# Optimization experiments

Hardware: AMD Instinct MI355X
Metric: run time of the kernel (lower is better)

## Reference

```python
import jax, jax.numpy as jnp
import numpy as np

N_NODES = 50000
W_IN = 256
W_OUT = 256
HEADS = 8
D_HEAD = W_OUT // HEADS
NUM_EDGE = 3
N_EDGES = 800000
NEG_SLOPE = 0.2


def setup_inputs() -> dict:
    key = jax.random.key(0)
    ks = jax.random.split(key, 10)
    x = jax.random.normal(ks[0], (N_NODES, W_IN), dtype=jnp.float32)
    adj = jax.random.randint(ks[1], (NUM_EDGE, 2, N_EDGES), 0, N_NODES, dtype=jnp.int64)
    sw = 1.0 / np.sqrt(W_IN)
    # Per-edge-type GATConv params, stacked on leading edge-type axis
    Ws = jax.random.normal(ks[2], (NUM_EDGE, W_IN, HEADS * D_HEAD), dtype=jnp.float32) * sw
    a_l = jax.random.normal(ks[3], (NUM_EDGE, HEADS, D_HEAD), dtype=jnp.float32) * 0.1
    a_r = jax.random.normal(ks[4], (NUM_EDGE, HEADS, D_HEAD), dtype=jnp.float32) * 0.1
    bias = jnp.zeros((NUM_EDGE, HEADS * D_HEAD), dtype=jnp.float32)
    # Semantic attention layer: Linear(w_out -> 1)
    att_w = jax.random.normal(ks[5], (W_OUT, 1), dtype=jnp.float32) * (1.0 / np.sqrt(W_OUT))
    att_b = jnp.zeros((1,), dtype=jnp.float32)
    return {"x": x, "adj": adj, "Ws": Ws, "a_l": a_l, "a_r": a_r,
            "bias": bias, "att_w": att_w, "att_b": att_b}


def _gat(x, edge_index, W, al, ar, b):
    # x: [N, W_IN]; edge_index: [2, E]; W: [W_IN, H*D]; al/ar: [H, D]; b: [H*D]
    N = x.shape[0]
    h = (x @ W).reshape(N, HEADS, D_HEAD)            # [N, H, D]
    src, dst = edge_index[0], edge_index[1]
    el = jnp.einsum('nhd,hd->nh', h, al)             # src-side scores [N, H]
    er = jnp.einsum('nhd,hd->nh', h, ar)             # dst-side scores [N, H]
    e = jax.nn.leaky_relu(el[src] + er[dst], NEG_SLOPE)   # [E, H]
    # segment softmax over incoming edges of each dst node
    m = jax.ops.segment_max(e, dst, num_segments=N)       # [N, H]
    e = jnp.exp(e - m[dst])
    s = jax.ops.segment_sum(e, dst, num_segments=N)       # [N, H]
    alpha = e / (s[dst] + 1e-9)                           # [E, H]
    out = jax.ops.segment_sum(alpha[:, :, None] * h[src], dst, num_segments=N)
    return out.reshape(N, HEADS * D_HEAD) + b             # concat heads [N, W_OUT]


def reference(x, adj, Ws, a_l, a_r, bias, att_w, att_b):
    outs = [_gat(x, adj[i], Ws[i], a_l[i], a_r[i], bias[i]) for i in range(NUM_EDGE)]
    stacked = jnp.stack(outs, axis=1)                     # [N, T, W_OUT]
    # AttentionLayer: scores = Linear(stacked) viewed as [N, 1, T]; NO softmax (faithful)
    att = (stacked @ att_w + att_b).reshape(-1, 1, NUM_EDGE)  # [N, 1, T]
    return jnp.matmul(att, stacked).squeeze(1)            # [N, W_OUT]
```

## Files before the change

### kernel.cpp

```cpp
#include <hip/hip_runtime.h>

#define N_NODES 50000
#define W_IN    256
#define W_OUT   256
#define HEADS   8
#define NUM_T   3
#define N_EDGES 800000
#define NEG_SLOPE 0.2f

#define NB      128
#define BSH     9
#define BNODES  512
#define P1_EPT  16
#define P1_CHUNK (256 * P1_EPT)
#define P1_BLOCKS ((N_EDGES + P1_CHUNK - 1) / P1_CHUNK)
#define NB_USED ((N_NODES + BNODES - 1) / BNODES)

typedef __attribute__((ext_vector_type(8))) short bf16x8;
typedef __attribute__((ext_vector_type(4))) float f32x4;

__device__ __forceinline__ unsigned short f2b(float f) {
    unsigned u = __float_as_uint(f);
    u = (u + 0x7fffu + ((u >> 16) & 1u)) >> 16;
    return (unsigned short)u;
}
__device__ __forceinline__ float blo(unsigned u) { return __uint_as_float(u << 16); }
__device__ __forceinline__ float bhi(unsigned u) { return __uint_as_float(u & 0xffff0000u); }

__global__ __launch_bounds__(256) void convert_x(const float* __restrict__ x,
                                                 unsigned short* __restrict__ xb) {
    const size_t i = ((size_t)blockIdx.x * 256 + threadIdx.x) * 4;
    const float4 v = *(const float4*)(x + i);
    ushort4 o;
    o.x = f2b(v.x); o.y = f2b(v.y); o.z = f2b(v.z); o.w = f2b(v.w);
    *(ushort4*)(xb + i) = o;
}

__global__ __launch_bounds__(256) void convert_W(const float* __restrict__ Wsrc,
                                                 unsigned short* __restrict__ Wt) {
    const int t = blockIdx.y;
    const int gid = blockIdx.x * 256 + threadIdx.x;
    const int k = gid >> 8, n = gid & 255;
    Wt[(size_t)t * 65536 + (size_t)n * 256 + k] = f2b(Wsrc[(size_t)t * 65536 + gid]);
}

__global__ __launch_bounds__(256) void p1_hist(const int* __restrict__ adj,
                                               int* __restrict__ bucket_cnt) {
    __shared__ int lh[NB];
    const int t = blockIdx.y;
    const int tid = threadIdx.x;
    if (tid < NB) lh[tid] = 0;
    __syncthreads();

    const int* dstp = adj + (size_t)t * 2 * N_EDGES + N_EDGES;
    const int e0 = blockIdx.x * P1_CHUNK + tid * P1_EPT;
#pragma unroll
    for (int i = 0; i < P1_EPT; ++i) {
        const int e = e0 + i;
        if (e < N_EDGES) atomicAdd(&lh[dstp[e] >> BSH], 1);
    }
    __syncthreads();
    if (tid < NB && lh[tid] > 0) atomicAdd(&bucket_cnt[t * NB + tid], lh[tid]);
}

__global__ __launch_bounds__(128) void p1_scan(const int* __restrict__ bucket_cnt,
                                               int* __restrict__ bucket_ptr,
                                               int* __restrict__ bucket_cur) {
    __shared__ int s[NB];
    const int tid = threadIdx.x;
    for (int t = 0; t < NUM_T; ++t) {
        const int v = bucket_cnt[t * NB + tid];
        s[tid] = v;
        __syncthreads();
        for (int off = 1; off < NB; off <<= 1) {
            int o = (tid >= off) ? s[tid - off] : 0;
            __syncthreads();
            s[tid] += o;
            __syncthreads();
        }
        const int incl = s[tid];
        const int excl = incl - v;
        bucket_ptr[t * (NB + 1) + tid] = excl;
        bucket_cur[t * NB + tid] = excl;
        if (tid == NB - 1) bucket_ptr[t * (NB + 1) + NB] = incl;
        __syncthreads();
    }
}

__global__ __launch_bounds__(256) void p1_scatter(const int* __restrict__ adj,
                                                  int* __restrict__ bucket_cur,
                                                  uint2* __restrict__ part) {
    __shared__ int lh[NB];
    __shared__ int lbase[NB];
    const int t = blockIdx.y;
    const int tid = threadIdx.x;
    if (tid < NB) lh[tid] = 0;
    __syncthreads();

    const int* srcp = adj + (size_t)t * 2 * N_EDGES;
    const int* dstp = srcp + N_EDGES;
    const int e0 = blockIdx.x * P1_CHUNK + tid * P1_EPT;

    int es[P1_EPT], ed[P1_EPT], rk[P1_EPT];
#pragma unroll
    for (int i = 0; i < P1_EPT; ++i) {
        const int e = e0 + i;
        if (e < N_EDGES) {
            es[i] = srcp[e];
            ed[i] = dstp[e];
            rk[i] = atomicAdd(&lh[ed[i] >> BSH], 1);
        } else {
            ed[i] = -1;
        }
    }
    __syncthreads();
    if (tid < NB && lh[tid] > 0)
        lbase[tid] = atomicAdd(&bucket_cur[t * NB + tid], lh[tid]);
    __syncthreads();

    uint2* pt = part + (size_t)t * N_EDGES;
#pragma unroll
    for (int i = 0; i < P1_EPT; ++i) {
        if (ed[i] >= 0) {
            const int b = ed[i] >> BSH;
            pt[lbase[b] + rk[i]] = make_uint2((unsigned)es[i], (unsigned)ed[i]);
        }
    }
}

__global__ __launch_bounds__(256) void p2_csr(const uint2* __restrict__ part,
                                              const int* __restrict__ bucket_ptr,
                                              int* __restrict__ row_ptr_all,
                                              int* __restrict__ csr_all) {
    __shared__ int sc[BNODES];
    const int b = blockIdx.x;
    const int t = blockIdx.y;
    const int tid = threadIdx.x;
    const int lane = tid & 63;
    const int wave = tid >> 6;

    const uint2* pt = part + (size_t)t * N_EDGES;
    int* row_ptr = row_ptr_all + (size_t)t * (N_NODES + 1);
    int* csr = csr_all + (size_t)t * N_EDGES;

    const int bp0 = bucket_ptr[t * (NB + 1) + b];
    const int bp1 = bucket_ptr[t * (NB + 1) + b + 1];
    const int node0 = b * BNODES;
    int nn = N_NODES - node0; if (nn > BNODES) nn = BNODES;

    sc[tid] = 0; sc[tid + 256] = 0;
    __syncthreads();

    for (int idx = bp0 + tid; idx < bp1; idx += 256)
        atomicAdd(&sc[pt[idx].y - node0], 1);
    __syncthreads();

    if (wave == 0) {
        int v[8], ex[8];
        int s = 0;
#pragma unroll
        for (int i = 0; i < 8; ++i) { v[i] = sc[lane * 8 + i]; ex[i] = s; s += v[i]; }
        int run = s;
        for (int off = 1; off < 64; off <<= 1) {
            int o = __shfl_up(run, off);
            if (lane >= off) run += o;
        }
        const int base = run - s;
#pragma unroll
        for (int i = 0; i < 8; ++i) sc[lane * 8 + i] = base + ex[i];
    }
    __syncthreads();

    for (int i = tid; i < nn; i += 256) row_ptr[node0 + i] = bp0 + sc[i];
    if (b == NB_USED - 1 && tid == 0) row_ptr[N_NODES] = N_EDGES;
    __syncthreads();

    for (int idx = bp0 + tid; idx < bp1; idx += 256) {
        const uint2 e = pt[idx];
        const int pos = bp0 + atomicAdd(&sc[e.y - node0], 1);
        csr[pos] = (int)e.x;
    }
}

__global__ __launch_bounds__(256) void gemm_fused(const unsigned short* __restrict__ xb,
                                                  const unsigned short* __restrict__ Wt,
                                                  const float* __restrict__ al,
                                                  const float* __restrict__ ar,
                                                  unsigned short* __restrict__ H,
                                                  float* __restrict__ el,
                                                  float* __restrict__ er) {
    __shared__ unsigned short As[64 * 40];
    __shared__ unsigned short Bs[256 * 40];
    __shared__ float els[64 * 8];
    __shared__ float ers[64 * 8];

    const int tid = threadIdx.x;
    const int wave = tid >> 6;
    const int lane = tid & 63;
    const int quad = lane >> 4;
    const int l16 = lane & 15;
    const int m0 = blockIdx.x * 64;

    f32x4 acc[4][4] = {};

    const int arow = tid >> 2;
    const int achunk = (tid & 3) * 8;
    int gm = m0 + arow;
    if (gm > N_NODES - 1) gm = N_NODES - 1;
    const unsigned short* aptr = xb + (size_t)gm * W_IN + achunk;

    for (int k0 = 0; k0 < W_IN; k0 += 32) {
        const uint4 av = *(const uint4*)(aptr + k0);
        *(uint4*)&As[arow * 40 + achunk] = av;
#pragma unroll
        for (int i = 0; i < 4; ++i) {
            const int idx = i * 256 + tid;
            const int brow = idx >> 2;
            const int bch = (idx & 3) * 8;
            const uint4 bv = *(const uint4*)(Wt + (size_t)brow * W_IN + k0 + bch);
            *(uint4*)&Bs[brow * 40 + bch] = bv;
        }
        __syncthreads();

        bf16x8 af[4], bfr[4];
#pragma unroll
        for (int mi = 0; mi < 4; ++mi)
            af[mi] = *(const bf16x8*)&As[(mi * 16 + l16) * 40 + quad * 8];
#pragma unroll
        for (int ni = 0; ni < 4; ++ni)
            bfr[ni] = *(const bf16x8*)&Bs[(wave * 64 + ni * 16 + l16) * 40 + quad * 8];
#pragma unroll
        for (int mi = 0; mi < 4; ++mi)
#pragma unroll
            for (int ni = 0; ni < 4; ++ni)
                acc[mi][ni] = __builtin_amdgcn_mfma_f32_16x16x32_bf16(
                    af[mi], bfr[ni], acc[mi][ni], 0, 0, 0);
        __syncthreads();
    }

#pragma unroll
    for (int mi = 0; mi < 4; ++mi)
#pragma unroll
        for (int reg = 0; reg < 4; ++reg) {
            const int gr = m0 + mi * 16 + quad * 4 + reg;
            if (gr < N_NODES)
#pragma unroll
                for (int ni = 0; ni < 4; ++ni)
                    H[(size_t)gr * W_OUT + wave * 64 + ni * 16 + l16] =
                        f2b(acc[mi][ni][reg]);
        }

    float al4[4], ar4[4];
#pragma unroll
    for (int ni = 0; ni < 4; ++ni) {
        const int c = wave * 64 + ni * 16 + l16;
        al4[ni] = al[c];
        ar4[ni] = ar[c];
    }
#pragma unroll
    for (int mi = 0; mi < 4; ++mi) {
        float pl[4][2] = {}, pr[4][2] = {};
#pragma unroll
        for (int ni = 0; ni < 4; ++ni) {
            const int hl = ni >> 1;
#pragma unroll
            for (int reg = 0; reg < 4; ++reg) {
                pl[reg][hl] += acc[mi][ni][reg] * al4[ni];
                pr[reg][hl] += acc[mi][ni][reg] * ar4[ni];
            }
        }
#pragma unroll
        for (int off = 1; off < 16; off <<= 1)
#pragma unroll
            for (int reg = 0; reg < 4; ++reg)
#pragma unroll
                for (int hl = 0; hl < 2; ++hl) {
                    pl[reg][hl] += __shfl_xor(pl[reg][hl], off);
                    pr[reg][hl] += __shfl_xor(pr[reg][hl], off);
                }
        if (l16 == 0)
#pragma unroll
            for (int reg = 0; reg < 4; ++reg)
#pragma unroll
                for (int hl = 0; hl < 2; ++hl) {
                    const int row = mi * 16 + quad * 4 + reg;
                    els[row * 8 + wave * 2 + hl] = pl[reg][hl];
                    ers[row * 8 + wave * 2 + hl] = pr[reg][hl];
                }
    }
    __syncthreads();

    int nn = N_NODES - m0; if (nn > 64) nn = 64;
    const int nn8 = nn * 8;
    const int i = tid * 4;
    if (i < nn8) {
        *(float4*)(el + (size_t)m0 * 8 + i) = *(float4*)&els[i];
        *(float4*)(er + (size_t)m0 * 8 + i) = *(float4*)&ers[i];
    }
}

__global__ __launch_bounds__(256) void gat_gather(const int* __restrict__ csr_src,
                                                  const int* __restrict__ row_ptr,
                                                  const float* __restrict__ el,
                                                  const float* __restrict__ er,
                                                  const unsigned short* __restrict__ H,
                                                  unsigned short* __restrict__ ot) {
    const int node = (blockIdx.x * blockDim.x + threadIdx.x) >> 6;
    const int lane = threadIdx.x & 63;
    if (node >= N_NODES) return;
    const int half = lane >> 5;
    const int d8 = lane & 31;
    const int hh = d8 >> 2;

    const int beg = row_ptr[node];
    const int end = row_ptr[node + 1];
    const float erv = er[(size_t)node * HEADS + hh];

    float acc[8] = {};
    float ssum = 0.f;

    for (int j0 = beg; j0 < end; j0 += 64) {
        int navail = end - j0;
        if (navail > 64) navail = 64;
        int mysrc = 0;
        if (j0 + lane < end) mysrc = csr_src[j0 + lane];

        const int npairs = (navail + 1) >> 1;
        for (int p = 0; p < npairs; ++p) {
            const int ei = 2 * p + half;
            const int src = __shfl(mysrc, ei);
            float v = el[(size_t)src * HEADS + hh] + erv;
            v = (v > 0.f) ? v : NEG_SLOPE * v;
            const float w = (ei < navail) ? __expf(v) : 0.f;
            const uint4 u = *(const uint4*)(H + (size_t)src * W_OUT + d8 * 8);
            acc[0] += w * blo(u.x);
            acc[1] += w * bhi(u.x);
            acc[2] += w * blo(u.y);
            acc[3] += w * bhi(u.y);
            acc[4] += w * blo(u.z);
            acc[5] += w * bhi(u.z);
            acc[6] += w * blo(u.w);
            acc[7] += w * bhi(u.w);
            ssum += w;
        }
    }

#pragma unroll
    for (int i = 0; i < 8; ++i) acc[i] += __shfl_xor(acc[i], 32);
    ssum += __shfl_xor(ssum, 32);

    if (half == 0) {
        const float inv = 1.f / (ssum + 1e-9f);
        unsigned short o8[8];
#pragma unroll
        for (int i = 0; i < 8; ++i) o8[i] = f2b(acc[i] * inv);
        *(uint4*)(ot + (size_t)node * W_OUT + d8 * 8) = *(const uint4*)o8;
    }
}

__global__ __launch_bounds__(256) void combine(const unsigned short* __restrict__ ot0,
                                               const unsigned short* __restrict__ ot1,
                                               const unsigned short* __restrict__ ot2,
                                               const float* __restrict__ bias,
                                               const float* __restrict__ att_w,
                                               const float* __restrict__ att_b,
                                               float* __restrict__ out) {
    const int gw = (blockIdx.x * blockDim.x + threadIdx.x) >> 6;
    const int lane = threadIdx.x & 63;
    if (gw >= N_NODES) return;

    const float4 aw = *(const float4*)(att_w + lane * 4);
    const size_t base = (size_t)gw * W_OUT + lane * 4;

    float4 v[NUM_T];
    float p[NUM_T];
    const unsigned short* ots[NUM_T] = {ot0, ot1, ot2};
#pragma unroll
    for (int t = 0; t < NUM_T; ++t) {
        const uint2 u = *(const uint2*)(ots[t] + base);
        const float4 bv = *(const float4*)(bias + t * W_OUT + lane * 4);
        float4 hv;
        hv.x = blo(u.x) + bv.x;
        hv.y = bhi(u.x) + bv.y;
        hv.z = blo(u.y) + bv.z;
        hv.w = bhi(u.y) + bv.w;
        v[t] = hv;
        p[t] = hv.x * aw.x + hv.y * aw.y + hv.z * aw.z + hv.w * aw.w;
    }
#pragma unroll
    for (int off = 1; off < 64; off <<= 1) {
        p[0] += __shfl_xor(p[0], off);
        p[1] += __shfl_xor(p[1], off);
        p[2] += __shfl_xor(p[2], off);
    }
    const float ab = att_b[0];
    const float a0 = p[0] + ab, a1 = p[1] + ab, a2 = p[2] + ab;
    float4 o;
    o.x = a0 * v[0].x + a1 * v[1].x + a2 * v[2].x;
    o.y = a0 * v[0].y + a1 * v[1].y + a2 * v[2].y;
    o.z = a0 * v[0].z + a1 * v[1].z + a2 * v[2].z;
    o.w = a0 * v[0].w + a1 * v[1].w + a2 * v[2].w;
    *(float4*)(out + base) = o;
}

extern "C" void kernel_launch(void* const* d_in, const int* in_sizes, int n_in,
                              void* d_out, int out_size, void* d_ws, size_t ws_size,
                              hipStream_t stream) {
    const float* x     = (const float*)d_in[0];
    const int*   adj   = (const int*)d_in[1];
    const float* Ws    = (const float*)d_in[2];
    const float* a_l   = (const float*)d_in[3];
    const float* a_r   = (const float*)d_in[4];
    const float* bias  = (const float*)d_in[5];
    const float* att_w = (const float*)d_in[6];
    const float* att_b = (const float*)d_in[7];
    float* out = (float*)d_out;

    char* w = (char*)d_ws;
    unsigned short* xb = (unsigned short*)w; w += (size_t)N_NODES * W_IN * 2;
    unsigned short* H  = (unsigned short*)w; w += (size_t)N_NODES * W_OUT * 2;
    unsigned short* Wt = (unsigned short*)w; w += (size_t)NUM_T * 65536 * 2;
    unsigned short* ot0 = (unsigned short*)w; w += (size_t)N_NODES * W_OUT * 2;
    unsigned short* ot1 = (unsigned short*)w; w += (size_t)N_NODES * W_OUT * 2;
    unsigned short* ot2 = (unsigned short*)w; w += (size_t)N_NODES * W_OUT * 2;
    float* el  = (float*)w; w += (size_t)N_NODES * HEADS * 4;
    float* er  = (float*)w; w += (size_t)N_NODES * HEADS * 4;
    int* csr_src = (int*)w; w += (size_t)NUM_T * N_EDGES * 4;
    int* row_ptr = (int*)w; w += (size_t)NUM_T * (N_NODES + 1) * 4;
    int* bucket_cnt = (int*)w; w += NUM_T * NB * 4;
    int* bucket_ptr = (int*)w; w += NUM_T * (NB + 1) * 4;
    int* bucket_cur = (int*)w; w += NUM_T * NB * 4;
    uint2* part = (uint2*)ot0;

    unsigned short* ot[NUM_T] = {ot0, ot1, ot2};
    const int node_wave_blocks = (N_NODES + 3) / 4;
    const int gemm_blocks = (N_NODES + 63) / 64;

    hipMemsetAsync(bucket_cnt, 0, NUM_T * NB * sizeof(int), stream);
    convert_x<<<12500, 256, 0, stream>>>(x, xb);
    convert_W<<<dim3(256, NUM_T), 256, 0, stream>>>(Ws, Wt);
    p1_hist<<<dim3(P1_BLOCKS, NUM_T), 256, 0, stream>>>(adj, bucket_cnt);
    p1_scan<<<1, 128, 0, stream>>>(bucket_cnt, bucket_ptr, bucket_cur);
    p1_scatter<<<dim3(P1_BLOCKS, NUM_T), 256, 0, stream>>>(adj, bucket_cur, part);
    p2_csr<<<dim3(NB_USED, NUM_T), 256, 0, stream>>>(part, bucket_ptr, row_ptr,
                                                     csr_src);

    for (int t = 0; t < NUM_T; ++t) {
        gemm_fused<<<gemm_blocks, 256, 0, stream>>>(
            xb, Wt + (size_t)t * 65536, a_l + t * 256, a_r + t * 256, H, el, er);
        gat_gather<<<node_wave_blocks, 256, 0, stream>>>(
            csr_src + (size_t)t * N_EDGES, row_ptr + (size_t)t * (N_NODES + 1),
            el, er, H, ot[t]);
    }

    combine<<<node_wave_blocks, 256, 0, stream>>>(ot0, ot1, ot2, bias, att_w,
                                                  att_b, out);
}
```

Measured before the change: 523.3 us.

## Stage bucket scatter in LDS and software-pipeline gather loads

The partition scatter now sorts each block's edges by bucket in shared memory using a wave-level prefix scan, then writes them out with contiguous, coalesced stores instead of scattered per-thread writes. The GAT gather loop is restructured to prefetch the next edge's H row and el value one iteration ahead, so global load latency overlaps with the current accumulation. The cost is 32KB of LDS per scatter block, which lowers occupancy, plus extra registers for the prefetched data in the gather kernel.

```diff
diff --git a/kernel.cpp b/kernel.cpp
--- a/kernel.cpp
+++ b/kernel.cpp
@@ -91,9 +91,13 @@
                                                   int* __restrict__ bucket_cur,
                                                   uint2* __restrict__ part) {
     __shared__ int lh[NB];
+    __shared__ int loff[NB];
     __shared__ int lbase[NB];
+    __shared__ uint2 buf[P1_CHUNK];
     const int t = blockIdx.y;
     const int tid = threadIdx.x;
+    const int lane = tid & 63;
+    const int wave = tid >> 6;
     if (tid < NB) lh[tid] = 0;
     __syncthreads();
 
@@ -114,17 +118,37 @@
         }
     }
     __syncthreads();
+
     if (tid < NB && lh[tid] > 0)
         lbase[tid] = atomicAdd(&bucket_cur[t * NB + tid], lh[tid]);
+    if (wave == 0) {
+        const int c0 = lh[lane * 2], c1 = lh[lane * 2 + 1];
+        const int s = c0 + c1;
+        int run = s;
+        for (int off = 1; off < 64; off <<= 1) {
+            const int o = __shfl_up(run, off);
+            if (lane >= off) run += o;
+        }
+        const int base = run - s;
+        loff[lane * 2] = base;
+        loff[lane * 2 + 1] = base + c0;
+    }
+    __syncthreads();
+
+#pragma unroll
+    for (int i = 0; i < P1_EPT; ++i)
+        if (ed[i] >= 0)
+            buf[loff[ed[i] >> BSH] + rk[i]] =
+                make_uint2((unsigned)es[i], (unsigned)ed[i]);
     __syncthreads();
 
     uint2* pt = part + (size_t)t * N_EDGES;
-#pragma unroll
-    for (int i = 0; i < P1_EPT; ++i) {
-        if (ed[i] >= 0) {
-            const int b = ed[i] >> BSH;
-            pt[lbase[b] + rk[i]] = make_uint2((unsigned)es[i], (unsigned)ed[i]);
-        }
+    int nvalid = N_EDGES - blockIdx.x * P1_CHUNK;
+    if (nvalid > P1_CHUNK) nvalid = P1_CHUNK;
+    for (int idx = tid; idx < nvalid; idx += 256) {
+        const uint2 e = buf[idx];
+        const int b = (int)(e.y >> BSH);
+        pt[lbase[b] + (idx - loff[b])] = e;
     }
 }
 
@@ -313,47 +337,59 @@
     const int hh = d8 >> 2;
 
     const int beg = row_ptr[node];
-    const int end = row_ptr[node + 1];
+    const int deg = row_ptr[node + 1] - beg;
     const float erv = er[(size_t)node * HEADS + hh];
 
-    float acc[8] = {};
+    float2 acc[4] = {};
     float ssum = 0.f;
 
-    for (int j0 = beg; j0 < end; j0 += 64) {
-        int navail = end - j0;
-        if (navail > 64) navail = 64;
-        int mysrc = 0;
-        if (j0 + lane < end) mysrc = csr_src[j0 + lane];
-
-        const int npairs = (navail + 1) >> 1;
-        for (int p = 0; p < npairs; ++p) {
-            const int ei = 2 * p + half;
-            const int src = __shfl(mysrc, ei);
-            float v = el[(size_t)src * HEADS + hh] + erv;
+    if (deg > 0) {
+        int mysrc = (lane < deg) ? csr_src[beg + lane] : 0;
+        const int npairs = (deg + 1) >> 1;
+
+        int src0 = __shfl(mysrc, half);
+        uint4 u0 = *(const uint4*)(H + (size_t)src0 * W_OUT + d8 * 8);
+        float elv0 = el[(size_t)src0 * HEADS + hh];
+
+        for (int q = 0; q < npairs; ++q) {
+            int src1 = 0; uint4 u1 = u0; float elv1 = 0.f;
+            const int q1 = q + 1;
+            if (q1 < npairs) {
+                if ((q1 & 31) == 0) {
+                    const int cb = beg + (q1 >> 5) * 64;
+                    mysrc = (cb + lane < beg + deg) ? csr_src[cb + lane] : 0;
+                }
+                src1 = __shfl(mysrc, (2 * q1 + half) & 63);
+                u1 = *(const uint4*)(H + (size_t)src1 * W_OUT + d8 * 8);
+                elv1 = el[(size_t)src1 * HEADS + hh];
+            }
+            float v = elv0 + erv;
             v = (v > 0.f) ? v : NEG_SLOPE * v;
-            const float w = (ei < navail) ? __expf(v) : 0.f;
-            const uint4 u = *(const uint4*)(H + (size_t)src * W_OUT + d8 * 8);
-            acc[0] += w * blo(u.x);
-            acc[1] += w * bhi(u.x);
-            acc[2] += w * blo(u.y);
-            acc[3] += w * bhi(u.y);
-            acc[4] += w * blo(u.z);
-            acc[5] += w * bhi(u.z);
-            acc[6] += w * blo(u.w);
-            acc[7] += w * bhi(u.w);
+            const float w = (2 * q + half < deg) ? __expf(v) : 0.f;
+            acc[0].x += w * blo(u0.x); acc[0].y += w * bhi(u0.x);
+            acc[1].x += w * blo(u0.y); acc[1].y += w * bhi(u0.y);
+            acc[2].x += w * blo(u0.z); acc[2].y += w * bhi(u0.z);
+            acc[3].x += w * blo(u0.w); acc[3].y += w * bhi(u0.w);
             ssum += w;
-        }
-    }
-
-#pragma unroll
-    for (int i = 0; i < 8; ++i) acc[i] += __shfl_xor(acc[i], 32);
+            src0 = src1; u0 = u1; elv0 = elv1;
+        }
+    }
+
+#pragma unroll
+    for (int i = 0; i < 4; ++i) {
+        acc[i].x += __shfl_xor(acc[i].x, 32);
+        acc[i].y += __shfl_xor(acc[i].y, 32);
+    }
     ssum += __shfl_xor(ssum, 32);
 
     if (half == 0) {
         const float inv = 1.f / (ssum + 1e-9f);
         unsigned short o8[8];
 #pragma unroll
-        for (int i = 0; i < 8; ++i) o8[i] = f2b(acc[i] * inv);
+        for (int i = 0; i < 4; ++i) {
+            o8[2 * i]     = f2b(acc[i].x * inv);
+            o8[2 * i + 1] = f2b(acc[i].y * inv);
+        }
         *(uint4*)(ot + (size_t)node * W_OUT + d8 * 8) = *(const uint4*)o8;
     }
 }
```

New measurement: 504.2 us. 1.04x faster.
